# Kernel tuning notes

Measured on AMD Instinct MI355X. Metric: run time of the kernel, lower is better.

## Reference

```python
import jax, jax.numpy as jnp
import numpy as np
from jax import lax

THR = 0.0
NMS_SIZE = 5
PAD = NMS_SIZE // 2
B, C, H, W = 8, 1, 2048, 2048
# Upper bound on number of surviving peaks: ~1/(2*25) of pixels pass in
# expectation for iid noise; B*H*W//8 is a very safe static cap.
MAX_PEAKS = (B * H * W) // 8


def max_filter(x):
    # torch MaxPool2d(kernel=5, stride=1, padding=2) == max reduce_window
    # with -inf padding, same spatial output shape.
    return lax.reduce_window(
        x, -jnp.inf, lax.max,
        window_dimensions=(1, 1, NMS_SIZE, NMS_SIZE),
        window_strides=(1, 1, 1, 1),
        padding=[(0, 0), (0, 0), (PAD, PAD), (PAD, PAD)],
    )


def setup_inputs() -> dict:
    key = jax.random.key(0)
    scores = jax.random.normal(key, (B, C, H, W), dtype=jnp.float32)
    return {"scores": scores}


def reference(scores):
    # maxima = (scores == maxpool(scores)) & (scores > thr)
    maxima = (scores == max_filter(scores)) & (scores > THR)
    # torch: maxima.nonzero().t()[2:4] -> [2, K] rows = (h, w) coords.
    # jit-safe: fixed-size nonzero, padded with -1 for absent entries.
    idx = jnp.nonzero(maxima, size=MAX_PEAKS, fill_value=-1)
    return jnp.stack([idx[2], idx[3]])  # [2, MAX_PEAKS]
```

## Files before the change

### kernel.cpp

```cpp
#include <hip/hip_runtime.h>
#include <math.h>

#define IMG_W 2048
#define IMG_H 2048
#define BATCH 8
#define MAX_PEAKS ((BATCH * IMG_H * IMG_W) / 8)
#define NWORDS (BATCH * IMG_H * IMG_W / 32)
#define ROWSW 32
#define NFILL 2048


#define NMS_COMPUTE(uu)                                                       \
  {                                                                           \
    const float4 w0 = ring[(uu) & 7];                                         \
    const float4 w1 = ring[((uu) + 1) & 7];                                   \
    const float4 mid = ring[((uu) + 2) & 7];                                  \
    const float4 w3 = ring[((uu) + 3) & 7];                                   \
    const float4 w4 = ring[((uu) + 4) & 7];                                   \
    float vmx = fmaxf(fmaxf(fmaxf(w0.x, w1.x), fmaxf(mid.x, w3.x)), w4.x);    \
    float vmy = fmaxf(fmaxf(fmaxf(w0.y, w1.y), fmaxf(mid.y, w3.y)), w4.y);    \
    float vmz = fmaxf(fmaxf(fmaxf(w0.z, w1.z), fmaxf(mid.z, w3.z)), w4.z);    \
    float vmw = fmaxf(fmaxf(fmaxf(w0.w, w1.w), fmaxf(mid.w, w3.w)), w4.w);    \
    const float2 e0 = ringE[(uu) & 7];                                        \
    const float2 e1 = ringE[((uu) + 1) & 7];                                  \
    const float2 e2 = ringE[((uu) + 2) & 7];                                  \
    const float2 e3 = ringE[((uu) + 3) & 7];                                  \
    const float2 e4 = ringE[((uu) + 4) & 7];                                  \
    float vex = fmaxf(fmaxf(fmaxf(e0.x, e1.x), fmaxf(e2.x, e3.x)), e4.x);     \
    float vey = fmaxf(fmaxf(fmaxf(e0.y, e1.y), fmaxf(e2.y, e3.y)), e4.y);     \
    float Av = __shfl_up(vmz, 1);                                             \
    float Bv = __shfl_up(vmw, 1);                                             \
    float Cv = __shfl_down(vmx, 1);                                           \
    float Dv = __shfl_down(vmy, 1);                                           \
    if (isL) { Av = vex; Bv = vey; }                                          \
    if (isR) { Cv = vex; Dv = vey; }                                          \
    float t12 = fmaxf(vmy, vmz);                                              \
    float m02 = fmaxf(vmx, t12);                                              \
    float m03 = fmaxf(m02, vmw);                                              \
    float m13 = fmaxf(t12, vmw);                                              \
    float h0 = fmaxf(fmaxf(Av, Bv), m02);                                     \
    float h1 = fmaxf(Bv, m03);                                                \
    float h2 = fmaxf(m03, Cv);                                                \
    float h3 = fmaxf(m13, fmaxf(Cv, Dv));                                     \
    unsigned nib = 0;                                                         \
    nib |= (mid.x > 0.0f && mid.x >= h0) ? 1u : 0u;                           \
    nib |= (mid.y > 0.0f && mid.y >= h1) ? 2u : 0u;                           \
    nib |= (mid.z > 0.0f && mid.z >= h2) ? 4u : 0u;                           \
    nib |= (mid.w > 0.0f && mid.w >= h3) ? 8u : 0u;                           \
    unsigned wd = nib << shamt;                                               \
    wd |= __shfl_xor(wd, 1);                                                  \
    wd |= __shfl_xor(wd, 2);                                                  \
    wd |= __shfl_xor(wd, 4);                                                  \
    if ((lane & 7) == 0) {                                                    \
      words[wIdx] = wd;                                                       \
      cnt += __popc(wd);                                                      \
    }                                                                         \
    wIdx += IMG_W / 32;                                                       \
  }

#define PF_FAST(uu)                                                           \
  {                                                                           \
    ring[((uu) + 7) & 7] = *(const float4*)p;                                 \
    const float2 _e = *(const float2*)pe;                                     \
    float2 _ne;                                                               \
    _ne.x = evalid ? _e.x : NEG;                                              \
    _ne.y = evalid ? _e.y : NEG;                                              \
    ringE[((uu) + 7) & 7] = _ne;                                              \
    p += IMG_W;                                                               \
    pe += IMG_W;                                                              \
  }

#define PF_SLOW(uu, gr)                                                       \
  {                                                                           \
    const int _rc = (gr) < 0 ? 0 : ((gr) > IMG_H - 1 ? IMG_H - 1 : (gr));     \
    const size_t _off = (size_t)_rc * IMG_W;                                  \
    const float4 _v = *(const float4*)(colp + _off);                          \
    const float2 _e = *(const float2*)(ecolp + _off);                         \
    const bool _rv = ((unsigned)(gr) < (unsigned)IMG_H);                      \
    const bool _ok = _rv && evalid;                                           \
    float4 _nv;                                                               \
    float2 _ne;                                                               \
    _nv.x = _rv ? _v.x : NEG;                                                 \
    _nv.y = _rv ? _v.y : NEG;                                                 \
    _nv.z = _rv ? _v.z : NEG;                                                 \
    _nv.w = _rv ? _v.w : NEG;                                                 \
    _ne.x = _ok ? _e.x : NEG;                                                 \
    _ne.y = _ok ? _e.y : NEG;                                                 \
    ring[((uu) + 7) & 7] = _nv;                                               \
    ringE[((uu) + 7) & 7] = _ne;                                              \
  }

#define FLUSH(k)                                                              \
  {                                                                           \
    unsigned s = cnt;                                                         \
    s += __shfl_xor(s, 1);                                                    \
    s += __shfl_xor(s, 2);                                                    \
    s += __shfl_xor(s, 4);                                                    \
    s += __shfl_xor(s, 8);                                                    \
    s += __shfl_xor(s, 16);                                                   \
    s += __shfl_xor(s, 32);                                                   \
    if (lane == 0) bsum2[(cb0 + (k)) * 8 + strip] = s;                        \
    cnt = 0;                                                                  \
  }

__global__ __launch_bounds__(256, 4) void nms_mask(const float* __restrict__ scores,
                                                   unsigned* __restrict__ words,
                                                   unsigned* __restrict__ bsum2) {
    const int t = threadIdx.x;
    const int lane = t & 63;
    const int wv = t >> 6;
    const int b = blockIdx.x;
    const int img = b >> 7;
    const int rem = b & 127;
    const int strip = rem >> 4;
    const int chunk = rem & 15;
    const int r0 = chunk * 128 + wv * ROWSW;
    const int c0 = strip * 256;
    const int cl = c0 + lane * 4;
    const size_t imgBase = (size_t)img * ((size_t)IMG_H * IMG_W);
    const float NEG = -INFINITY;

    const float* colp = scores + imgBase + cl;
    const bool leftHalf = (lane < 32);
    const bool isL = (lane == 0), isR = (lane == 63);
    const int ecol2 = leftHalf ? (c0 - 2) : (c0 + 256);
    const bool evalid = ((unsigned)ecol2 < (unsigned)IMG_W);
    const int ecol2C = evalid ? ecol2 : c0;
    const float* ecolp = scores + imgBase + ecol2C;

    float4 ring[8];
    float2 ringE[8];

    unsigned cnt = 0;
    const int shamt = (lane & 7) * 4;
    size_t wIdx = (size_t)(img * IMG_H + r0) * (IMG_W / 32) + strip * 8 + (lane >> 3);
    const int cb0 = (img * IMG_H + r0) >> 4;

    const bool rowsInterior = (r0 >= 2) && (r0 + 33 <= IMG_H - 1);

    if (rowsInterior) {
        const float* p = colp + (size_t)(r0 - 2) * IMG_W;
        const float* pe = ecolp + (size_t)(r0 - 2) * IMG_W;
#pragma unroll
        for (int m = 0; m < 7; ++m) {
            ring[m] = *(const float4*)p;
            const float2 _e = *(const float2*)pe;
            ringE[m].x = evalid ? _e.x : NEG;
            ringE[m].y = evalid ? _e.y : NEG;
            p += IMG_W;
            pe += IMG_W;
        }
#pragma unroll 1
        for (int i8 = 0; i8 < 2; ++i8) {
#pragma unroll
            for (int uu = 0; uu < 8; ++uu) {
                PF_FAST(uu);
                NMS_COMPUTE(uu);
            }
        }
        FLUSH(0);
#pragma unroll
        for (int uu = 0; uu < 8; ++uu) {
            PF_FAST(uu);
            NMS_COMPUTE(uu);
        }
#pragma unroll
        for (int uu = 0; uu < 5; ++uu) {
            PF_FAST(uu);
            NMS_COMPUTE(uu);
        }
#pragma unroll
        for (int uu = 5; uu < 8; ++uu) {
            NMS_COMPUTE(uu);
        }
        FLUSH(1);
    } else {
#pragma unroll
        for (int m = 0; m < 7; ++m) {
            PF_SLOW(m - 7, r0 - 2 + m);
        }
#pragma unroll 1
        for (int i8 = 0; i8 < 4; ++i8) {
#pragma unroll
            for (int uu = 0; uu < 8; ++uu) {
                const int U = i8 * 8 + uu;
                PF_SLOW(uu, r0 + U + 5);
                NMS_COMPUTE(uu);
            }
            if (i8 & 1) FLUSH(i8 >> 1);
        }
    }
}

__global__ __launch_bounds__(256) void nms_scan(const unsigned* __restrict__ bsum2,
                                                unsigned* __restrict__ base) {
    __shared__ unsigned wtot[4];
    const int t = threadIdx.x;
    const int lane = t & 63, wid = t >> 6;
    const uint4* p = (const uint4*)(bsum2 + t * 32);
    unsigned c[4];
#pragma unroll
    for (int i = 0; i < 4; ++i) {
        uint4 a = p[2 * i], bq = p[2 * i + 1];
        c[i] = a.x + a.y + a.z + a.w + bq.x + bq.y + bq.z + bq.w;
    }
    unsigned s0 = c[0], s1 = s0 + c[1], s2 = s1 + c[2], ts = s2 + c[3];
    unsigned sc = ts;
#pragma unroll
    for (int d = 1; d < 64; d <<= 1) {
        unsigned o = __shfl_up(sc, d);
        if (lane >= d) sc += o;
    }
    if (lane == 63) wtot[wid] = sc;
    __syncthreads();
    unsigned wpre = 0;
#pragma unroll
    for (int k = 0; k < 4; ++k) wpre += (k < wid) ? wtot[k] : 0u;
    unsigned excl = wpre + sc - ts;
    ((uint4*)base)[t] = make_uint4(excl, excl + s0, excl + s1, excl + s2);
    if (t == 255) base[1024] = wpre + sc;
}

__global__ __launch_bounds__(256) void nms_compact(const unsigned* __restrict__ words,
                                                   const unsigned* __restrict__ base,
                                                   int* __restrict__ out) {
    const int t = threadIdx.x;
    const int b = blockIdx.x;
    if (b < 1024) {
        __shared__ unsigned wq[4];
        const int lane = t & 63, wid = t >> 6;
        uint4 q = ((const uint4*)(words + b * 1024))[t];
        unsigned wv[4] = {q.x, q.y, q.z, q.w};
        unsigned tsum = __popc(wv[0]) + __popc(wv[1]) + __popc(wv[2]) + __popc(wv[3]);
        unsigned sc = tsum;
#pragma unroll
        for (int d = 1; d < 64; d <<= 1) {
            unsigned o = __shfl_up(sc, d);
            if (lane >= d) sc += o;
        }
        if (lane == 63) wq[wid] = sc;
        __syncthreads();
        unsigned wpre = 0;
#pragma unroll
        for (int k = 0; k < 4; ++k) wpre += (k < wid) ? wq[k] : 0u;
        unsigned off = base[b] + wpre + sc - tsum;

        const unsigned gword0 = (unsigned)b * 1024u + (unsigned)t * 4u;
#pragma unroll
        for (int wi = 0; wi < 4; ++wi) {
            unsigned m = wv[wi];
            unsigned pbase = (gword0 + wi) << 5;
            while (m) {
                int bit = __builtin_ctz(m);
                m &= m - 1;
                unsigned ppix = pbase + (unsigned)bit;
                int hh = (int)((ppix >> 11) & 2047u);
                int ww = (int)(ppix & 2047u);
                if (off < (unsigned)MAX_PEAKS) {
                    out[off] = hh;
                    out[MAX_PEAKS + off] = ww;
                }
                ++off;
            }
        }
    } else {
        unsigned total = base[1024];
        if (total > (unsigned)MAX_PEAKS) total = MAX_PEAKS;
        unsigned tail = (unsigned)MAX_PEAKS - total;
        unsigned fb = (unsigned)(b - 1024);
        unsigned per = (tail + NFILL - 1) / NFILL;
        unsigned s = total + fb * per;
        unsigned e = s + per;
        if (s > (unsigned)MAX_PEAKS) s = MAX_PEAKS;
        if (e > (unsigned)MAX_PEAKS) e = MAX_PEAKS;
        unsigned a = (s + 3u) & ~3u;
        if (a > e) a = e;
        unsigned e4 = e & ~3u;
        if (e4 < a) e4 = a;
        if ((unsigned)t < a - s) {
            out[s + t] = -1;
            out[MAX_PEAKS + s + t] = -1;
        }
        const int4 m4 = make_int4(-1, -1, -1, -1);
        for (unsigned k = a / 4 + t; k < e4 / 4; k += 256) {
            ((int4*)out)[k] = m4;
            ((int4*)(out + MAX_PEAKS))[k] = m4;
        }
        if ((unsigned)t < e - e4) {
            out[e4 + t] = -1;
            out[MAX_PEAKS + e4 + t] = -1;
        }
    }
}

extern "C" void kernel_launch(void* const* d_in, const int* in_sizes, int n_in,
                              void* d_out, int out_size, void* d_ws, size_t ws_size,
                              hipStream_t stream) {
    const float* scores = (const float*)d_in[0];
    int* out = (int*)d_out;
    unsigned* words = (unsigned*)d_ws;
    unsigned* bsum2 = words + NWORDS;
    unsigned* base = bsum2 + 8192;

    nms_mask<<<1024, 256, 0, stream>>>(scores, words, bsum2);
    nms_scan<<<1, 256, 0, stream>>>(bsum2, base);
    nms_compact<<<1024 + NFILL, 256, 0, stream>>>(words, base, out);
}
```

Before: 213.4 us.

## Fuse scan into compact kernel and batch nibble merges per eight rows

Drops the single-block scan kernel. Each compact block now sums the prefix of block counts itself by reading up to 8192 partial sums, which removes one launch and its serialization point. In the mask kernel, per-row nibbles are gathered into a 32-bit accumulator and merged with shuffles once every eight rows, so shuffles and stores are grouped instead of interleaved with each row's compute. The cost is redundant prefix reads in every compact block, averaging about 16 KB and up to 32 KB each across 3072 blocks.

After: 256.9 us. 1.2x slower.

```diff
diff --git a/kernel.cpp b/kernel.cpp
--- a/kernel.cpp
+++ b/kernel.cpp
@@ -47,15 +47,22 @@
     nib |= (mid.y > 0.0f && mid.y >= h1) ? 2u : 0u;                           \
     nib |= (mid.z > 0.0f && mid.z >= h2) ? 4u : 0u;                           \
     nib |= (mid.w > 0.0f && mid.w >= h3) ? 8u : 0u;                           \
-    unsigned wd = nib << shamt;                                               \
-    wd |= __shfl_xor(wd, 1);                                                  \
-    wd |= __shfl_xor(wd, 2);                                                  \
-    wd |= __shfl_xor(wd, 4);                                                  \
-    if ((lane & 7) == 0) {                                                    \
-      words[wIdx] = wd;                                                       \
-      cnt += __popc(wd);                                                      \
+    bacc |= nib << (4 * (uu));                                                \
+  }
+
+#define MERGE8(i8v, bb)                                                       \
+  {                                                                           \
+    _Pragma("unroll")                                                         \
+    for (int q = 0; q < 8; ++q) {                                             \
+      unsigned wd = (((bb) >> (q * 4)) & 0xFu) << shamt;                      \
+      wd |= __shfl_xor(wd, 1);                                                \
+      wd |= __shfl_xor(wd, 2);                                                \
+      wd |= __shfl_xor(wd, 4);                                                \
+      if ((lane & 7) == 0) {                                                  \
+        words[wRow + (size_t)((i8v) * 8 + q) * (IMG_W / 32)] = wd;            \
+        cnt += __popc(wd);                                                    \
+      }                                                                       \
     }                                                                         \
-    wIdx += IMG_W / 32;                                                       \
   }
 
 #define PF_FAST(uu)                                                           \
@@ -133,7 +140,7 @@
 
     unsigned cnt = 0;
     const int shamt = (lane & 7) * 4;
-    size_t wIdx = (size_t)(img * IMG_H + r0) * (IMG_W / 32) + strip * 8 + (lane >> 3);
+    const size_t wRow = (size_t)(img * IMG_H + r0) * (IMG_W / 32) + strip * 8 + (lane >> 3);
     const int cb0 = (img * IMG_H + r0) >> 4;
 
     const bool rowsInterior = (r0 >= 2) && (r0 + 33 <= IMG_H - 1);
@@ -152,26 +159,36 @@
         }
 #pragma unroll 1
         for (int i8 = 0; i8 < 2; ++i8) {
+            unsigned bacc = 0;
 #pragma unroll
             for (int uu = 0; uu < 8; ++uu) {
                 PF_FAST(uu);
                 NMS_COMPUTE(uu);
             }
+            MERGE8(i8, bacc);
         }
         FLUSH(0);
-#pragma unroll
-        for (int uu = 0; uu < 8; ++uu) {
-            PF_FAST(uu);
-            NMS_COMPUTE(uu);
-        }
-#pragma unroll
-        for (int uu = 0; uu < 5; ++uu) {
-            PF_FAST(uu);
-            NMS_COMPUTE(uu);
-        }
-#pragma unroll
-        for (int uu = 5; uu < 8; ++uu) {
-            NMS_COMPUTE(uu);
+        {
+            unsigned bacc = 0;
+#pragma unroll
+            for (int uu = 0; uu < 8; ++uu) {
+                PF_FAST(uu);
+                NMS_COMPUTE(uu);
+            }
+            MERGE8(2, bacc);
+        }
+        {
+            unsigned bacc = 0;
+#pragma unroll
+            for (int uu = 0; uu < 5; ++uu) {
+                PF_FAST(uu);
+                NMS_COMPUTE(uu);
+            }
+#pragma unroll
+            for (int uu = 5; uu < 8; ++uu) {
+                NMS_COMPUTE(uu);
+            }
+            MERGE8(3, bacc);
         }
         FLUSH(1);
     } else {
@@ -181,54 +198,46 @@
         }
 #pragma unroll 1
         for (int i8 = 0; i8 < 4; ++i8) {
+            unsigned bacc = 0;
 #pragma unroll
             for (int uu = 0; uu < 8; ++uu) {
                 const int U = i8 * 8 + uu;
                 PF_SLOW(uu, r0 + U + 5);
                 NMS_COMPUTE(uu);
             }
+            MERGE8(i8, bacc);
             if (i8 & 1) FLUSH(i8 >> 1);
         }
     }
 }
 
-__global__ __launch_bounds__(256) void nms_scan(const unsigned* __restrict__ bsum2,
-                                                unsigned* __restrict__ base) {
-    __shared__ unsigned wtot[4];
-    const int t = threadIdx.x;
-    const int lane = t & 63, wid = t >> 6;
-    const uint4* p = (const uint4*)(bsum2 + t * 32);
-    unsigned c[4];
-#pragma unroll
-    for (int i = 0; i < 4; ++i) {
-        uint4 a = p[2 * i], bq = p[2 * i + 1];
-        c[i] = a.x + a.y + a.z + a.w + bq.x + bq.y + bq.z + bq.w;
-    }
-    unsigned s0 = c[0], s1 = s0 + c[1], s2 = s1 + c[2], ts = s2 + c[3];
-    unsigned sc = ts;
-#pragma unroll
-    for (int d = 1; d < 64; d <<= 1) {
-        unsigned o = __shfl_up(sc, d);
-        if (lane >= d) sc += o;
-    }
-    if (lane == 63) wtot[wid] = sc;
-    __syncthreads();
-    unsigned wpre = 0;
-#pragma unroll
-    for (int k = 0; k < 4; ++k) wpre += (k < wid) ? wtot[k] : 0u;
-    unsigned excl = wpre + sc - ts;
-    ((uint4*)base)[t] = make_uint4(excl, excl + s0, excl + s1, excl + s2);
-    if (t == 255) base[1024] = wpre + sc;
-}
-
 __global__ __launch_bounds__(256) void nms_compact(const unsigned* __restrict__ words,
-                                                   const unsigned* __restrict__ base,
+                                                   const unsigned* __restrict__ bsum2,
                                                    int* __restrict__ out) {
     const int t = threadIdx.x;
     const int b = blockIdx.x;
+    const int lane = t & 63, wid = t >> 6;
+    __shared__ unsigned sred[4];
+    __shared__ unsigned wq[4];
+
+    const int limq = ((b < 1024) ? (b * 8) : 8192) >> 2;
+    unsigned acc = 0;
+    const uint4* p4 = (const uint4*)bsum2;
+    for (int i = t; i < limq; i += 256) {
+        uint4 a = p4[i];
+        acc += a.x + a.y + a.z + a.w;
+    }
+    acc += __shfl_xor(acc, 1);
+    acc += __shfl_xor(acc, 2);
+    acc += __shfl_xor(acc, 4);
+    acc += __shfl_xor(acc, 8);
+    acc += __shfl_xor(acc, 16);
+    acc += __shfl_xor(acc, 32);
+    if (lane == 0) sred[wid] = acc;
+    __syncthreads();
+    const unsigned basev = sred[0] + sred[1] + sred[2] + sred[3];
+
     if (b < 1024) {
-        __shared__ unsigned wq[4];
-        const int lane = t & 63, wid = t >> 6;
         uint4 q = ((const uint4*)(words + b * 1024))[t];
         unsigned wv[4] = {q.x, q.y, q.z, q.w};
         unsigned tsum = __popc(wv[0]) + __popc(wv[1]) + __popc(wv[2]) + __popc(wv[3]);
@@ -243,7 +252,7 @@
         unsigned wpre = 0;
 #pragma unroll
         for (int k = 0; k < 4; ++k) wpre += (k < wid) ? wq[k] : 0u;
-        unsigned off = base[b] + wpre + sc - tsum;
+        unsigned off = basev + wpre + sc - tsum;
 
         const unsigned gword0 = (unsigned)b * 1024u + (unsigned)t * 4u;
 #pragma unroll
@@ -264,7 +273,7 @@
             }
         }
     } else {
-        unsigned total = base[1024];
+        unsigned total = basev;
         if (total > (unsigned)MAX_PEAKS) total = MAX_PEAKS;
         unsigned tail = (unsigned)MAX_PEAKS - total;
         unsigned fb = (unsigned)(b - 1024);
@@ -300,9 +309,7 @@
     int* out = (int*)d_out;
     unsigned* words = (unsigned*)d_ws;
     unsigned* bsum2 = words + NWORDS;
-    unsigned* base = bsum2 + 8192;
 
     nms_mask<<<1024, 256, 0, stream>>>(scores, words, bsum2);
-    nms_scan<<<1, 256, 0, stream>>>(bsum2, base);
-    nms_compact<<<1024 + NFILL, 256, 0, stream>>>(words, base, out);
+    nms_compact<<<1024 + NFILL, 256, 0, stream>>>(words, bsum2, out);
 }
```
